# Kernel tuning notes

Measured on AMD Instinct MI355X. Metric: run time of the kernel, lower is better.

Reference implementation:

```python
import jax, jax.numpy as jnp
import numpy as np

N_NODES = 50000


def setup_inputs() -> dict:
    key = jax.random.key(0)
    k1, k2, k3, k4 = jax.random.split(key, 4)
    in_c, hid = 256, 128
    x = jax.random.normal(k1, (N_NODES, in_c), dtype=jnp.float32)
    edge_index = jax.random.randint(k2, (2, 800000), 0, N_NODES, dtype=jnp.int32)
    # GCNConv weight (glorot) and bias
    W_conv = jax.random.normal(k3, (in_c, hid), dtype=jnp.float32) * (1.0 / np.sqrt(in_c))
    b_conv = jnp.zeros((hid,), dtype=jnp.float32)
    # Final Linear (xavier_uniform per reset_parameters)
    limit = np.sqrt(6.0 / (hid + in_c))
    W_lin = jax.random.uniform(k4, (hid, in_c), dtype=jnp.float32, minval=-limit, maxval=limit)
    b_lin = jnp.zeros((in_c,), dtype=jnp.float32)
    return {"x": x, "edge_index": edge_index, "W_conv": W_conv, "b_conv": b_conv,
            "W_lin": W_lin, "b_lin": b_lin}


def _gcn_conv(x, edge_index, W, b):
    n = x.shape[0]
    # add self-loops (standard GCN normalization)
    loop = jnp.arange(n, dtype=edge_index.dtype)
    src = jnp.concatenate([edge_index[0], loop])
    dst = jnp.concatenate([edge_index[1], loop])
    # transform first (in_c -> hid) so the edge gather moves the smaller dim
    h = x @ W  # [N, hid]
    deg = jax.ops.segment_sum(jnp.ones_like(dst, dtype=h.dtype), dst, num_segments=n)
    dinv = jnp.where(deg > 0, jax.lax.rsqrt(deg), 0.0)
    norm = dinv[src] * dinv[dst]  # [E+N]
    msg = h[src] * norm[:, None]  # [E+N, hid]
    out = jax.ops.segment_sum(msg, dst, num_segments=n)
    return out + b


def reference(x, edge_index, W_conv, b_conv, W_lin, b_lin):
    h = _gcn_conv(x, edge_index, W_conv, b_conv)  # [N, hid]
    # dropout p=0.0 -> identity
    return h @ W_lin + b_lin  # [N, in_c]
```

## Files before the change

### kernel.cpp

```cpp
#include <hip/hip_runtime.h>
#include <hip/hip_fp16.h>


#define N_NODES 50000
#define N_EDGES 800000
#define IN_C 256
#define HID 128
#define SCAN_BLOCKS ((N_NODES + 255) / 256)
#define GEMM_MBLK ((N_NODES + 63) / 64)
#define PREP_BLOCKS 1024
#define LDK 72

#define OFF_H    0UL
#define OFF_CONV 12800000UL
#define OFF_DEG  25600000UL
#define OFF_RP   25800000UL
#define OFF_DINV 26000064UL
#define OFF_RANK 26200064UL
#define OFF_REC  27800064UL
#define OFF_BSUM 31000064UL
#define OFF_WT1  31001088UL
#define OFF_WT2  31066624UL

typedef __attribute__((ext_vector_type(8))) short bf16x8;
typedef __attribute__((ext_vector_type(4))) float f32x4;

__device__ __forceinline__ ushort f2bf(float x) {
    unsigned u = __float_as_uint(x);
    u += 0x7fffu + ((u >> 16) & 1u);
    return (ushort)(u >> 16);
}

__global__ __launch_bounds__(256) void prep_kernel(
    const float* __restrict__ Wc, const float* __restrict__ Wl,
    ushort* __restrict__ wtc, ushort* __restrict__ wtl,
    const int* __restrict__ dst, ushort* __restrict__ rank, int* __restrict__ deg)
{
    int i = blockIdx.x * 256 + threadIdx.x;
    if (i < HID * IN_C) {
        int n = i / IN_C, k = i % IN_C;
        wtc[i] = f2bf(Wc[k * HID + n]);
    } else if (i < 2 * HID * IN_C) {
        int j = i - HID * IN_C;
        int n = j / HID, k = j % HID;
        wtl[j] = f2bf(Wl[k * IN_C + n]);
    }
    for (int e = i; e < N_EDGES; e += PREP_BLOCKS * 256)
        rank[e] = (ushort)atomicAdd(&deg[dst[e]], 1);
}

__global__ __launch_bounds__(256) void scan_blocks_kernel(
    const int* __restrict__ deg, int* __restrict__ row_ptr,
    int* __restrict__ bsums, int n)
{
    __shared__ int tmp[256];
    int tid = threadIdx.x;
    int i = blockIdx.x * 256 + tid;
    int v = (i < n) ? deg[i] : 0;
    int orig = v;
    tmp[tid] = v;
    __syncthreads();
    #pragma unroll
    for (int off = 1; off < 256; off <<= 1) {
        int t = (tid >= off) ? tmp[tid - off] : 0;
        __syncthreads();
        tmp[tid] += t;
        __syncthreads();
    }
    if (i < n) row_ptr[i] = tmp[tid] - orig;
    if (tid == 255) bsums[blockIdx.x] = tmp[255];
}

__global__ __launch_bounds__(256) void finalize2_kernel(
    const int* __restrict__ deg, int* __restrict__ row_ptr,
    const int* __restrict__ bsums, float* __restrict__ dinv, int n)
{
    __shared__ int tmp[256];
    __shared__ int orig[256];
    int tid = threadIdx.x;
    int v = (tid < SCAN_BLOCKS) ? bsums[tid] : 0;
    tmp[tid] = v;
    orig[tid] = v;
    __syncthreads();
    #pragma unroll
    for (int off = 1; off < 256; off <<= 1) {
        int t = (tid >= off) ? tmp[tid - off] : 0;
        __syncthreads();
        tmp[tid] += t;
        __syncthreads();
    }
    int boff = tmp[blockIdx.x] - orig[blockIdx.x];
    int i = blockIdx.x * 256 + tid;
    if (i < n) {
        row_ptr[i] += boff;
        dinv[i] = rsqrtf((float)(deg[i] + 1));
    }
    if (i == 0) row_ptr[n] = N_EDGES;
}

#define BUCKET_BLOCKS 2048
__global__ __launch_bounds__(256) void bucket_kernel(
    const int* __restrict__ src, const int* __restrict__ dst,
    const ushort* __restrict__ rank, const int* __restrict__ row_ptr,
    const float* __restrict__ dinv, unsigned* __restrict__ rec)
{
    int cls = blockIdx.x & 7;
    int blk = blockIdx.x >> 3;
    int lo = cls * (N_NODES / 8);
    int hi = lo + (N_NODES / 8);
    const int CHUNK = (N_EDGES + 255) / 256;
    int e0 = blk * CHUNK;
    int e1 = min(e0 + CHUNK, N_EDGES);
    for (int i = e0 + threadIdx.x; i < e1; i += 256) {
        int d = dst[i];
        if (d >= lo && d < hi) {
            int s = src[i];
            unsigned r = (unsigned)(ushort)s |
                         ((unsigned)__half_as_ushort(__float2half_rn(dinv[s])) << 16);
            rec[row_ptr[d] + rank[i]] = r;
        }
    }
}

template <bool A_IS_BF16, bool BF16OUT>
__global__ __launch_bounds__(256) void mfma_gemm_kernel(
    const void* __restrict__ Av, const ushort* __restrict__ Bt,
    const float* __restrict__ bias, void* __restrict__ Cv,
    int M, int N, int K)
{
    __shared__ __align__(16) ushort As[64 * LDK];
    __shared__ __align__(16) ushort Bs[128 * LDK];
    int tid = threadIdx.x;
    int wave = tid >> 6, lane = tid & 63;
    int quad = lane >> 4, l16 = lane & 15;
    int wm0 = (wave >> 1) * 32, wn0 = (wave & 1) * 64;
    int bm = blockIdx.x * 64, bn = blockIdx.y * 128;

    f32x4 acc[2][4] = {};

    for (int k0 = 0; k0 < K; k0 += 64) {
        {
            int row = tid >> 2, col = (tid & 3) * 16;
            int grow = bm + row;
            if (A_IS_BF16) {
                bf16x8 v0 = {}, v1 = {};
                if (grow < M) {
                    const ushort* ap = (const ushort*)Av + (size_t)grow * K + k0 + col;
                    v0 = *(const bf16x8*)ap;
                    v1 = *(const bf16x8*)(ap + 8);
                }
                *(bf16x8*)&As[row * LDK + col]     = v0;
                *(bf16x8*)&As[row * LDK + col + 8] = v1;
            } else {
                float4 v0 = {}, v1 = {}, v2 = {}, v3 = {};
                if (grow < M) {
                    const float* ap = (const float*)Av + (size_t)grow * K + k0 + col;
                    v0 = *(const float4*)ap;
                    v1 = *(const float4*)(ap + 4);
                    v2 = *(const float4*)(ap + 8);
                    v3 = *(const float4*)(ap + 12);
                }
                ushort t0[8] = {f2bf(v0.x), f2bf(v0.y), f2bf(v0.z), f2bf(v0.w),
                                f2bf(v1.x), f2bf(v1.y), f2bf(v1.z), f2bf(v1.w)};
                ushort t1[8] = {f2bf(v2.x), f2bf(v2.y), f2bf(v2.z), f2bf(v2.w),
                                f2bf(v3.x), f2bf(v3.y), f2bf(v3.z), f2bf(v3.w)};
                *(bf16x8*)&As[row * LDK + col]     = *(bf16x8*)t0;
                *(bf16x8*)&As[row * LDK + col + 8] = *(bf16x8*)t1;
            }
        }
        {
            int n = tid >> 1;
            int kk = (tid & 1) * 32;
            const ushort* bp = Bt + (size_t)(bn + n) * K + k0 + kk;
            *(bf16x8*)&Bs[n * LDK + kk]      = *(const bf16x8*)bp;
            *(bf16x8*)&Bs[n * LDK + kk + 8]  = *(const bf16x8*)(bp + 8);
            *(bf16x8*)&Bs[n * LDK + kk + 16] = *(const bf16x8*)(bp + 16);
            *(bf16x8*)&Bs[n * LDK + kk + 24] = *(const bf16x8*)(bp + 24);
        }
        __syncthreads();
        bf16x8 af[2][2], bfr[4][2];
        #pragma unroll
        for (int im = 0; im < 2; ++im)
            #pragma unroll
            for (int kh = 0; kh < 2; ++kh)
                af[im][kh] = *(bf16x8*)&As[(wm0 + im * 16 + l16) * LDK + kh * 32 + quad * 8];
        #pragma unroll
        for (int in = 0; in < 4; ++in)
            #pragma unroll
            for (int kh = 0; kh < 2; ++kh)
                bfr[in][kh] = *(bf16x8*)&Bs[(wn0 + in * 16 + l16) * LDK + kh * 32 + quad * 8];
        #pragma unroll
        for (int im = 0; im < 2; ++im)
            #pragma unroll
            for (int in = 0; in < 4; ++in) {
                acc[im][in] = __builtin_amdgcn_mfma_f32_16x16x32_bf16(
                    af[im][0], bfr[in][0], acc[im][in], 0, 0, 0);
                acc[im][in] = __builtin_amdgcn_mfma_f32_16x16x32_bf16(
                    af[im][1], bfr[in][1], acc[im][in], 0, 0, 0);
            }
        __syncthreads();
    }
    #pragma unroll
    for (int im = 0; im < 2; ++im) {
        #pragma unroll
        for (int in = 0; in < 4; ++in) {
            int col = bn + wn0 + in * 16 + l16;
            float bval = bias ? bias[col] : 0.f;
            #pragma unroll
            for (int r = 0; r < 4; ++r) {
                int grow = bm + wm0 + im * 16 + quad * 4 + r;
                if (grow < M) {
                    float o = acc[im][in][r] + bval;
                    if (BF16OUT)
                        ((ushort*)Cv)[(size_t)grow * N + col] = f2bf(o);
                    else
                        ((float*)Cv)[(size_t)grow * N + col] = o;
                }
            }
        }
    }
}

__device__ __forceinline__ void acc_edge(float4& acc, unsigned r,
                                         const ushort* __restrict__ hb, int c) {
    unsigned s = r & 0xffffu;
    float w = __half2float(__ushort_as_half((ushort)(r >> 16)));
    uint2 v = *(const uint2*)&hb[(size_t)s * HID + c];
    acc.x += w * __uint_as_float(v.x << 16);
    acc.y += w * __uint_as_float(v.x & 0xffff0000u);
    acc.z += w * __uint_as_float(v.y << 16);
    acc.w += w * __uint_as_float(v.y & 0xffff0000u);
}

__global__ __launch_bounds__(256) void gather_kernel(
    const ushort* __restrict__ hb, const int* __restrict__ row_ptr,
    const unsigned* __restrict__ rec, const float* __restrict__ dinv,
    const float* __restrict__ b_conv, ushort* __restrict__ convb, int n)
{
    int wave = threadIdx.x >> 6;
    int lane = threadIdx.x & 63;
    int d = blockIdx.x * 4 + wave;
    if (d >= n) return;
    int half = lane >> 5;
    int l32 = lane & 31;
    int c = l32 << 2;

    float4 acc = make_float4(0.f, 0.f, 0.f, 0.f);
    int begin = row_ptr[d], end = row_ptr[d + 1];
    int e = begin + half;
    for (; e + 6 < end; e += 8) {
        unsigned r0 = rec[e];
        unsigned r1 = rec[e + 2];
        unsigned r2 = rec[e + 4];
        unsigned r3 = rec[e + 6];
        acc_edge(acc, r0, hb, c);
        acc_edge(acc, r1, hb, c);
        acc_edge(acc, r2, hb, c);
        acc_edge(acc, r3, hb, c);
    }
    for (; e < end; e += 2) {
        unsigned r0 = rec[e];
        acc_edge(acc, r0, hb, c);
    }
    acc.x += __shfl_xor(acc.x, 32);
    acc.y += __shfl_xor(acc.y, 32);
    acc.z += __shfl_xor(acc.z, 32);
    acc.w += __shfl_xor(acc.w, 32);

    if (half == 0) {
        float di = dinv[d];
        uint2 hv = *(const uint2*)&hb[(size_t)d * HID + c];
        acc.x += di * __uint_as_float(hv.x << 16);
        acc.y += di * __uint_as_float(hv.x & 0xffff0000u);
        acc.z += di * __uint_as_float(hv.y << 16);
        acc.w += di * __uint_as_float(hv.y & 0xffff0000u);
        float4 bb = *(const float4*)&b_conv[c];
        float ox = di * acc.x + bb.x;
        float oy = di * acc.y + bb.y;
        float oz = di * acc.z + bb.z;
        float ow = di * acc.w + bb.w;
        uint2 po;
        po.x = ((unsigned)f2bf(oy) << 16) | (unsigned)f2bf(ox);
        po.y = ((unsigned)f2bf(ow) << 16) | (unsigned)f2bf(oz);
        *(uint2*)&convb[(size_t)d * HID + c] = po;
    }
}

extern "C" void kernel_launch(void* const* d_in, const int* in_sizes, int n_in,
                              void* d_out, int out_size, void* d_ws, size_t ws_size,
                              hipStream_t stream) {
    const float* x      = (const float*)d_in[0];
    const int*   ei     = (const int*)d_in[1];
    const float* W_conv = (const float*)d_in[2];
    const float* b_conv = (const float*)d_in[3];
    const float* W_lin  = (const float*)d_in[4];
    const float* b_lin  = (const float*)d_in[5];
    float* out = (float*)d_out;

    char* ws = (char*)d_ws;
    ushort* hb      = (ushort*)(ws + OFF_H);
    ushort* convb   = (ushort*)(ws + OFF_CONV);
    int*    deg     = (int*)(ws + OFF_DEG);
    int*    row_ptr = (int*)(ws + OFF_RP);
    float*  dinv    = (float*)(ws + OFF_DINV);
    ushort* rank    = (ushort*)(ws + OFF_RANK);
    unsigned* rec   = (unsigned*)(ws + OFF_REC);
    int*    bsums   = (int*)(ws + OFF_BSUM);
    ushort* wt_conv = (ushort*)(ws + OFF_WT1);
    ushort* wt_lin  = (ushort*)(ws + OFF_WT2);

    const int* src = ei;
    const int* dst = ei + N_EDGES;

    hipMemsetAsync(deg, 0, 200000, stream);

    prep_kernel<<<PREP_BLOCKS, 256, 0, stream>>>(W_conv, W_lin, wt_conv, wt_lin,
                                                 dst, rank, deg);
    scan_blocks_kernel<<<SCAN_BLOCKS, 256, 0, stream>>>(deg, row_ptr, bsums, N_NODES);
    finalize2_kernel<<<SCAN_BLOCKS, 256, 0, stream>>>(deg, row_ptr, bsums, dinv, N_NODES);
    bucket_kernel<<<BUCKET_BLOCKS, 256, 0, stream>>>(src, dst, rank, row_ptr, dinv, rec);

    mfma_gemm_kernel<false, true><<<dim3(GEMM_MBLK, HID / 128), 256, 0, stream>>>(
        x, wt_conv, nullptr, hb, N_NODES, HID, IN_C);

    gather_kernel<<<(N_NODES + 3) / 4, 256, 0, stream>>>(
        hb, row_ptr, rec, dinv, b_conv, convb, N_NODES);

    mfma_gemm_kernel<true, false><<<dim3(GEMM_MBLK, IN_C / 128), 256, 0, stream>>>(
        convb, wt_lin, b_lin, out, N_NODES, IN_C, HID);
}
```

Before: 230.5 us.

## Fuse first GEMM and edge bucketing into one heterogeneous kernel launch

Merges the x@W_conv MFMA GEMM and the CSR bucket-fill pass into a single launch in which the first GEMM_MBLK blocks run GEMM tiles and the rest scatter edge records. The bucket pass now uses 1024 blocks instead of 2048, with each block covering twice as many edges. The aim is to overlap the compute-bound GEMM with the memory-bound scatter and drop one launch plus its serialization gap. In exchange, every block reserves GEMM shared memory even when doing bucket work, which may limit occupancy for the scatter blocks.

```diff
diff --git a/kernel.cpp b/kernel.cpp
--- a/kernel.cpp
+++ b/kernel.cpp
@@ -9,6 +9,7 @@
 #define SCAN_BLOCKS ((N_NODES + 255) / 256)
 #define GEMM_MBLK ((N_NODES + 63) / 64)
 #define PREP_BLOCKS 1024
+#define BUCKET_BLOCKS 1024
 #define LDK 72
 
 #define OFF_H    0UL
@@ -98,43 +99,17 @@
     if (i == 0) row_ptr[n] = N_EDGES;
 }
 
-#define BUCKET_BLOCKS 2048
-__global__ __launch_bounds__(256) void bucket_kernel(
-    const int* __restrict__ src, const int* __restrict__ dst,
-    const ushort* __restrict__ rank, const int* __restrict__ row_ptr,
-    const float* __restrict__ dinv, unsigned* __restrict__ rec)
-{
-    int cls = blockIdx.x & 7;
-    int blk = blockIdx.x >> 3;
-    int lo = cls * (N_NODES / 8);
-    int hi = lo + (N_NODES / 8);
-    const int CHUNK = (N_EDGES + 255) / 256;
-    int e0 = blk * CHUNK;
-    int e1 = min(e0 + CHUNK, N_EDGES);
-    for (int i = e0 + threadIdx.x; i < e1; i += 256) {
-        int d = dst[i];
-        if (d >= lo && d < hi) {
-            int s = src[i];
-            unsigned r = (unsigned)(ushort)s |
-                         ((unsigned)__half_as_ushort(__float2half_rn(dinv[s])) << 16);
-            rec[row_ptr[d] + rank[i]] = r;
-        }
-    }
-}
-
 template <bool A_IS_BF16, bool BF16OUT>
-__global__ __launch_bounds__(256) void mfma_gemm_kernel(
+__device__ __forceinline__ void gemm_tile_body(
     const void* __restrict__ Av, const ushort* __restrict__ Bt,
     const float* __restrict__ bias, void* __restrict__ Cv,
-    int M, int N, int K)
-{
-    __shared__ __align__(16) ushort As[64 * LDK];
-    __shared__ __align__(16) ushort Bs[128 * LDK];
+    int M, int N, int K, int bx, int by, ushort* As, ushort* Bs)
+{
     int tid = threadIdx.x;
     int wave = tid >> 6, lane = tid & 63;
     int quad = lane >> 4, l16 = lane & 15;
     int wm0 = (wave >> 1) * 32, wn0 = (wave & 1) * 64;
-    int bm = blockIdx.x * 64, bn = blockIdx.y * 128;
+    int bm = bx * 64, bn = by * 128;
 
     f32x4 acc[2][4] = {};
 
@@ -221,6 +196,52 @@
     }
 }
 
+template <bool A_IS_BF16, bool BF16OUT>
+__global__ __launch_bounds__(256) void mfma_gemm_kernel(
+    const void* __restrict__ Av, const ushort* __restrict__ Bt,
+    const float* __restrict__ bias, void* __restrict__ Cv,
+    int M, int N, int K)
+{
+    __shared__ __align__(16) ushort As[64 * LDK];
+    __shared__ __align__(16) ushort Bs[128 * LDK];
+    gemm_tile_body<A_IS_BF16, BF16OUT>(Av, Bt, bias, Cv, M, N, K,
+                                       blockIdx.x, blockIdx.y, As, Bs);
+}
+
+__global__ __launch_bounds__(256) void gemm1_bucket_kernel(
+    const float* __restrict__ x, const ushort* __restrict__ wt_conv,
+    ushort* __restrict__ hb,
+    const int* __restrict__ src, const int* __restrict__ dst,
+    const ushort* __restrict__ rank, const int* __restrict__ row_ptr,
+    const float* __restrict__ dinv, unsigned* __restrict__ rec)
+{
+    __shared__ __align__(16) ushort As[64 * LDK];
+    __shared__ __align__(16) ushort Bs[128 * LDK];
+    int bid = blockIdx.x;
+    if (bid < GEMM_MBLK) {
+        gemm_tile_body<false, true>(x, wt_conv, nullptr, hb,
+                                    N_NODES, HID, IN_C, bid, 0, As, Bs);
+    } else {
+        int bblk = bid - GEMM_MBLK;
+        int cls = (bblk + (GEMM_MBLK & 7)) & 7;
+        int blk = bblk >> 3;
+        int lo = cls * (N_NODES / 8);
+        int hi = lo + (N_NODES / 8);
+        const int CHUNK = (N_EDGES + 127) / 128;
+        int e0 = blk * CHUNK;
+        int e1 = min(e0 + CHUNK, N_EDGES);
+        for (int i = e0 + threadIdx.x; i < e1; i += 256) {
+            int d = dst[i];
+            if (d >= lo && d < hi) {
+                int s = src[i];
+                unsigned r = (unsigned)(ushort)s |
+                             ((unsigned)__half_as_ushort(__float2half_rn(dinv[s])) << 16);
+                rec[row_ptr[d] + rank[i]] = r;
+            }
+        }
+    }
+}
+
 __device__ __forceinline__ void acc_edge(float4& acc, unsigned r,
                                          const ushort* __restrict__ hb, int c) {
     unsigned s = r & 0xffffu;
@@ -318,10 +339,9 @@
                                                  dst, rank, deg);
     scan_blocks_kernel<<<SCAN_BLOCKS, 256, 0, stream>>>(deg, row_ptr, bsums, N_NODES);
     finalize2_kernel<<<SCAN_BLOCKS, 256, 0, stream>>>(deg, row_ptr, bsums, dinv, N_NODES);
-    bucket_kernel<<<BUCKET_BLOCKS, 256, 0, stream>>>(src, dst, rank, row_ptr, dinv, rec);
-
-    mfma_gemm_kernel<false, true><<<dim3(GEMM_MBLK, HID / 128), 256, 0, stream>>>(
-        x, wt_conv, nullptr, hb, N_NODES, HID, IN_C);
+
+    gemm1_bucket_kernel<<<GEMM_MBLK + BUCKET_BLOCKS, 256, 0, stream>>>(
+        x, wt_conv, hb, src, dst, rank, row_ptr, dinv, rec);
 
     gather_kernel<<<(N_NODES + 3) / 4, 256, 0, stream>>>(
         hb, row_ptr, rec, dinv, b_conv, convb, N_NODES);
```

After: 232.8 us. About the same (+1.0%).
